# Kernel tuning notes

Hardware: AMD Instinct MI355X
Metric: run time of the kernel (lower is better)

The kernel has to match this reference:

```python
import jax, jax.numpy as jnp
import numpy as np

NEG_BIG = -9e15
ALPHA = 0.2  # LeakyReLU negative slope


def setup_inputs() -> dict:
    key = jax.random.key(0)
    k1, k2, k3, k4 = jax.random.split(key, 4)
    N, Fin, Fout = 8192, 256, 256
    input_ = jax.random.normal(k1, (N, Fin), dtype=jnp.float32)
    adj = jax.random.randint(k2, (N, N), 0, 2, dtype=jnp.int32)
    # xavier_uniform with gain=1.414
    limW = 1.414 * np.sqrt(6.0 / (Fin + Fout))
    W = jax.random.uniform(k3, (Fin, Fout), minval=-limW, maxval=limW, dtype=jnp.float32)
    lima = 1.414 * np.sqrt(6.0 / (2 * Fout + 1))
    a = jax.random.uniform(k4, (2 * Fout, 1), minval=-lima, maxval=lima, dtype=jnp.float32)
    return {"input_": input_, "adj": adj, "W": W, "a": a}


def reference(input_, adj, W, a):
    # h: [N, F]
    h = input_ @ W
    F = h.shape[1]
    # Decompose cat([h_i, h_j]) @ a into per-node projections summed by broadcast
    src = h @ a[:F, 0]   # [N]  contribution of row node i
    dst = h @ a[F:, 0]   # [N]  contribution of col node j
    e = jax.nn.leaky_relu(src[:, None] + dst[None, :], negative_slope=ALPHA)  # [N, N]
    e = jnp.where(adj > 0, e, NEG_BIG)
    attention = jax.nn.softmax(e, axis=1)
    h_prime = attention @ h  # [N, F]
    return jax.nn.relu(h_prime)  # concat=True
```

## Files before the change

### kernel.cpp

```cpp
#include <hip/hip_runtime.h>
#include <math.h>

#define NN 8192
#define FF 256
#define ALPHA 0.2f
#define JT 32
#define LP 40

typedef __bf16 bf16x8 __attribute__((ext_vector_type(8)));
typedef float  f32x4  __attribute__((ext_vector_type(4)));

__global__ __launch_bounds__(256) void k1_xw(const float* __restrict__ X,
                                             const float* __restrict__ W,
                                             float* __restrict__ h) {
    __shared__ float xs[32][FF];
    const int t = threadIdx.x;
    const int i0 = blockIdx.x * 32;
    #pragma unroll
    for (int it = 0; it < 8; ++it) {
        int f = it * 256 + t;
        int r = f >> 6;
        int c4 = (f & 63) << 2;
        *(float4*)&xs[r][c4] = *(const float4*)&X[(size_t)(i0 + r) * FF + c4];
    }
    __syncthreads();
    float acc[32];
    #pragma unroll
    for (int r = 0; r < 32; ++r) acc[r] = 0.f;
    for (int kt = 0; kt < FF; kt += 8) {
        float wk[8];
        #pragma unroll
        for (int u = 0; u < 8; ++u) wk[u] = W[(size_t)(kt + u) * FF + t];
        #pragma unroll
        for (int r = 0; r < 32; ++r) {
            float4 xa = *(float4*)&xs[r][kt];
            float4 xb = *(float4*)&xs[r][kt + 4];
            acc[r] += xa.x * wk[0] + xa.y * wk[1] + xa.z * wk[2] + xa.w * wk[3]
                    + xb.x * wk[4] + xb.y * wk[5] + xb.z * wk[6] + xb.w * wk[7];
        }
    }
    #pragma unroll
    for (int r = 0; r < 32; ++r) h[(size_t)(i0 + r) * FF + t] = acc[r];
}

__global__ __launch_bounds__(256) void k1b_split(const float* __restrict__ h,
                                                 __bf16* __restrict__ hT) {
    __shared__ float ts[64][65];
    const int t = threadIdx.x;
    const int j0 = blockIdx.x * 64;
    const int f0 = blockIdx.y * 64;
    #pragma unroll
    for (int r = 0; r < 4; ++r) {
        int jr = r * 16 + (t >> 4);
        int fc = (t & 15) * 4;
        *(float4*)&ts[jr][fc] = *(const float4*)&h[(size_t)(j0 + jr) * FF + f0 + fc];
    }
    __syncthreads();
    const int f = t >> 2;
    const int jc = (t & 3) * 16;
    union { bf16x8 v[2]; __bf16 e[16]; } hi, lo;
    #pragma unroll
    for (int u = 0; u < 16; ++u) {
        float x = ts[jc + u][f];
        __bf16 h1 = (__bf16)x;
        hi.e[u] = h1;
        lo.e[u] = (__bf16)(x - (float)h1);
    }
    size_t base = (size_t)(f0 + f) * NN + j0 + jc;
    *(bf16x8*)&hT[base]     = hi.v[0];
    *(bf16x8*)&hT[base + 8] = hi.v[1];
    size_t lbase = (size_t)FF * NN + base;
    *(bf16x8*)&hT[lbase]     = lo.v[0];
    *(bf16x8*)&hT[lbase + 8] = lo.v[1];
}

__global__ __launch_bounds__(256) void k2_srcdst(const float* __restrict__ h,
                                                 const float* __restrict__ a,
                                                 float* __restrict__ src,
                                                 float* __restrict__ dst) {
    const int wv = threadIdx.x >> 6;
    const int l = threadIdx.x & 63;
    const int i = blockIdx.x * 4 + wv;
    float s = 0.f, d = 0.f;
    #pragma unroll
    for (int k = 0; k < 4; ++k) {
        float hv = h[(size_t)i * FF + l + 64 * k];
        s += hv * a[l + 64 * k];
        d += hv * a[FF + l + 64 * k];
    }
    #pragma unroll
    for (int off = 32; off > 0; off >>= 1) {
        s += __shfl_down(s, off);
        d += __shfl_down(d, off);
    }
    if (l == 0) { src[i] = s; dst[i] = d; }
}

__global__ __launch_bounds__(256) void k2b_max(const float* __restrict__ dst,
                                               float* __restrict__ maxd) {
    __shared__ float red[256];
    float m = -1e30f;
    for (int i = threadIdx.x; i < NN; i += 256) m = fmaxf(m, dst[i]);
    red[threadIdx.x] = m;
    __syncthreads();
    for (int s = 128; s > 0; s >>= 1) {
        if (threadIdx.x < s) red[threadIdx.x] = fmaxf(red[threadIdx.x], red[threadIdx.x + s]);
        __syncthreads();
    }
    if (threadIdx.x == 0) maxd[0] = red[0];
}

__global__ __launch_bounds__(256) void k3_attn(const int* __restrict__ adj,
                                               const __bf16* __restrict__ hT,
                                               const float* __restrict__ src,
                                               const float* __restrict__ dst,
                                               const float* __restrict__ maxd,
                                               float* __restrict__ num,
                                               float* __restrict__ den,
                                               int S) {
    __shared__ __bf16 bh[2][FF][LP];
    __shared__ __bf16 wA[64][LP];
    __shared__ float dl[64][4];
    const int t = threadIdx.x;
    const int nIt = NN / 64;
    const int it = blockIdx.x % nIt;
    const int seg = blockIdx.x / nIt;
    const int i0 = it * 64;
    const int jseg = NN / S;
    const int jbeg = seg * jseg;
    const int p_i = t >> 2;
    const int p_q = t & 3;
    const float maxdv = maxd[0];
    const float src_r = src[i0 + p_i];
    const float e0 = src_r + maxdv;
    const float m_r = e0 > 0.f ? e0 : ALPHA * e0;
    float den_reg = 0.f;
    const int wv = t >> 6;
    const int l = t & 63;
    const int ln = l & 15;
    const int g = l >> 4;
    f32x4 acc[4][4];
    #pragma unroll
    for (int mt = 0; mt < 4; ++mt)
        #pragma unroll
        for (int nt = 0; nt < 4; ++nt)
            acc[mt][nt] = (f32x4){0.f, 0.f, 0.f, 0.f};

    for (int jt = 0; jt < jseg; jt += JT) {
        const int j0 = jbeg + jt;
        __syncthreads();
        #pragma unroll
        for (int r = 0; r < 8; ++r) {
            int c = t + r * 256;
            int jc = c & 3;
            int f = (c >> 2) & 255;
            int hl = c >> 10;
            bf16x8 v = *(const bf16x8*)&hT[((size_t)hl * FF + f) * NN + j0 + jc * 8];
            *(bf16x8*)&bh[hl][f][jc * 8] = v;
        }
        {
            const int* ap = adj + (size_t)(i0 + p_i) * NN + j0 + p_q * 8;
            const int4 a0 = *(const int4*)ap;
            const int4 a1 = *(const int4*)(ap + 4);
            const float* dp = dst + j0 + p_q * 8;
            const float4 d0 = *(const float4*)dp;
            const float4 d1 = *(const float4*)(dp + 4);
            const int av[8] = {a0.x, a0.y, a0.z, a0.w, a1.x, a1.y, a1.z, a1.w};
            const float dv[8] = {d0.x, d0.y, d0.z, d0.w, d1.x, d1.y, d1.z, d1.w};
            union { bf16x8 v; __bf16 e[8]; } wu;
            #pragma unroll
            for (int u = 0; u < 8; ++u) {
                float e = src_r + dv[u];
                e = e > 0.f ? e : ALPHA * e;
                float w = (av[u] > 0) ? __expf(e - m_r) : 0.f;
                den_reg += w;
                wu.e[u] = (__bf16)w;
            }
            *(bf16x8*)&wA[p_i][p_q * 8] = wu.v;
        }
        __syncthreads();
        bf16x8 af[4];
        #pragma unroll
        for (int mt = 0; mt < 4; ++mt) af[mt] = *(bf16x8*)&wA[mt * 16 + ln][g * 8];
        #pragma unroll
        for (int nt = 0; nt < 4; ++nt) {
            #pragma unroll
            for (int hl = 0; hl < 2; ++hl) {
                bf16x8 bfr = *(bf16x8*)&bh[hl][wv * 64 + nt * 16 + ln][g * 8];
                #pragma unroll
                for (int mt = 0; mt < 4; ++mt)
                    acc[mt][nt] = __builtin_amdgcn_mfma_f32_16x16x32_bf16(
                        af[mt], bfr, acc[mt][nt], 0, 0, 0);
            }
        }
    }
    #pragma unroll
    for (int mt = 0; mt < 4; ++mt)
        #pragma unroll
        for (int nt = 0; nt < 4; ++nt)
            #pragma unroll
            for (int rg = 0; rg < 4; ++rg)
                num[((size_t)seg * NN + i0 + mt * 16 + g * 4 + rg) * FF
                    + wv * 64 + nt * 16 + ln] = acc[mt][nt][rg];
    dl[p_i][p_q] = den_reg;
    __syncthreads();
    if (t < 64) den[(size_t)seg * NN + i0 + t] = dl[t][0] + dl[t][1] + dl[t][2] + dl[t][3];
}

__global__ __launch_bounds__(256) void k4_out(const float* __restrict__ num,
                                              const float* __restrict__ den,
                                              float* __restrict__ out, int S) {
    size_t f4 = (size_t)blockIdx.x * 256 + threadIdx.x;
    int i = (int)(f4 >> 6);
    int c4 = (int)(f4 & 63) << 2;
    float4 s = make_float4(0.f, 0.f, 0.f, 0.f);
    float d = 0.f;
    for (int sg = 0; sg < S; ++sg) {
        float4 v = *(const float4*)&num[((size_t)sg * NN + i) * FF + c4];
        s.x += v.x; s.y += v.y; s.z += v.z; s.w += v.w;
        d += den[(size_t)sg * NN + i];
    }
    float inv = 1.f / d;
    float4 o;
    o.x = fmaxf(s.x * inv, 0.f);
    o.y = fmaxf(s.y * inv, 0.f);
    o.z = fmaxf(s.z * inv, 0.f);
    o.w = fmaxf(s.w * inv, 0.f);
    *(float4*)&out[(size_t)i * FF + c4] = o;
}

extern "C" void kernel_launch(void* const* d_in, const int* in_sizes, int n_in,
                              void* d_out, int out_size, void* d_ws, size_t ws_size,
                              hipStream_t stream) {
    const float* X  = (const float*)d_in[0];
    const int*  adj = (const int*)d_in[1];
    const float* W  = (const float*)d_in[2];
    const float* a  = (const float*)d_in[3];
    float* out = (float*)d_out;
    char* ws = (char*)d_ws;

    const size_t off_h    = 0;
    const size_t off_hT   = off_h + (size_t)NN * FF * 4;
    const size_t off_src  = off_hT + (size_t)2 * FF * NN * 2;
    const size_t off_dst  = off_src + (size_t)NN * 4;
    const size_t off_maxd = off_dst + (size_t)NN * 4;
    const size_t off_num  = off_maxd + 256;

    int S = 8;
    while (S > 1) {
        size_t need = off_num + (size_t)S * NN * FF * 4 + (size_t)S * NN * 4;
        if (need <= ws_size) break;
        S >>= 1;
    }
    const size_t off_den = off_num + (size_t)S * NN * FF * 4;

    float* h_ws   = (float*)(ws + off_h);
    __bf16* hT_ws = (__bf16*)(ws + off_hT);
    float* src_ws = (float*)(ws + off_src);
    float* dst_ws = (float*)(ws + off_dst);
    float* maxd   = (float*)(ws + off_maxd);
    float* num_ws = (float*)(ws + off_num);
    float* den_ws = (float*)(ws + off_den);

    k1_xw<<<NN / 32, 256, 0, stream>>>(X, W, h_ws);
    k1b_split<<<dim3(NN / 64, FF / 64), 256, 0, stream>>>(h_ws, hT_ws);
    k2_srcdst<<<NN / 4, 256, 0, stream>>>(h_ws, a, src_ws, dst_ws);
    k2b_max<<<1, 256, 0, stream>>>(dst_ws, maxd);
    k3_attn<<<(NN / 64) * S, 256, 0, stream>>>(adj, hT_ws, src_ws, dst_ws, maxd,
                                               num_ws, den_ws, S);
    k4_out<<<(NN * FF / 4) / 256, 256, 0, stream>>>(num_ws, den_ws, out, S);
}
```

Measured before the change: 540.7 us.

## Fuse projection into MFMA kernel and double-buffer attention loads via LDS DMA

Replaces the scalar XW matmul, the transpose/split and the src/dst kernels with one kernel. It computes h using split-bf16 MFMA and emits hT, src and dst directly. The attention kernel now double-buffers hT tiles in LDS through global_load_lds with a swizzled layout, prefetches the adjacency and dst values for the next step, and fixes the split count at 4 with launch_bounds occupancy 2. The aim is to remove extra launches, the fp32 round trip of h and load latency in the main loop. In exchange, the fixed split count ignores the workspace size, and the bf16 three-term projection changes numerics slightly.

Measured after the change: 481.9 us. 1.12x faster.

```diff
diff --git a/kernel.cpp b/kernel.cpp
--- a/kernel.cpp
+++ b/kernel.cpp
@@ -4,103 +4,178 @@
 #define NN 8192
 #define FF 256
 #define ALPHA 0.2f
-#define JT 32
-#define LP 40
+#define SS 4
+#define JSEG (NN / SS)
+#define STEPS (JSEG / 32)
 
 typedef __bf16 bf16x8 __attribute__((ext_vector_type(8)));
+typedef __bf16 bf16x4 __attribute__((ext_vector_type(4)));
 typedef float  f32x4  __attribute__((ext_vector_type(4)));
 
-__global__ __launch_bounds__(256) void k1_xw(const float* __restrict__ X,
-                                             const float* __restrict__ W,
-                                             float* __restrict__ h) {
-    __shared__ float xs[32][FF];
-    const int t = threadIdx.x;
-    const int i0 = blockIdx.x * 32;
-    #pragma unroll
-    for (int it = 0; it < 8; ++it) {
-        int f = it * 256 + t;
-        int r = f >> 6;
-        int c4 = (f & 63) << 2;
-        *(float4*)&xs[r][c4] = *(const float4*)&X[(size_t)(i0 + r) * FF + c4];
-    }
-    __syncthreads();
-    float acc[32];
-    #pragma unroll
-    for (int r = 0; r < 32; ++r) acc[r] = 0.f;
-    for (int kt = 0; kt < FF; kt += 8) {
-        float wk[8];
-        #pragma unroll
-        for (int u = 0; u < 8; ++u) wk[u] = W[(size_t)(kt + u) * FF + t];
-        #pragma unroll
-        for (int r = 0; r < 32; ++r) {
-            float4 xa = *(float4*)&xs[r][kt];
-            float4 xb = *(float4*)&xs[r][kt + 4];
-            acc[r] += xa.x * wk[0] + xa.y * wk[1] + xa.z * wk[2] + xa.w * wk[3]
-                    + xb.x * wk[4] + xb.y * wk[5] + xb.z * wk[6] + xb.w * wk[7];
-        }
-    }
-    #pragma unroll
-    for (int r = 0; r < 32; ++r) h[(size_t)(i0 + r) * FF + t] = acc[r];
-}
-
-__global__ __launch_bounds__(256) void k1b_split(const float* __restrict__ h,
-                                                 __bf16* __restrict__ hT) {
+__device__ __forceinline__ void dma16(const void* g, void* l) {
+    __builtin_amdgcn_global_load_lds((const __attribute__((address_space(1))) void*)g,
+                                     (__attribute__((address_space(3))) void*)l,
+                                     16, 0, 0);
+}
+
+__global__ __launch_bounds__(256) void k0_wt(const float* __restrict__ W,
+                                             __bf16* __restrict__ WT) {
     __shared__ float ts[64][65];
     const int t = threadIdx.x;
-    const int j0 = blockIdx.x * 64;
-    const int f0 = blockIdx.y * 64;
+    const int k0 = blockIdx.x * 64;
+    const int n0 = blockIdx.y * 64;
     #pragma unroll
     for (int r = 0; r < 4; ++r) {
-        int jr = r * 16 + (t >> 4);
-        int fc = (t & 15) * 4;
-        *(float4*)&ts[jr][fc] = *(const float4*)&h[(size_t)(j0 + jr) * FF + f0 + fc];
+        int krow = r * 16 + (t >> 4);
+        int nc4 = (t & 15) * 4;
+        *(float4*)&ts[krow][nc4] = *(const float4*)&W[(size_t)(k0 + krow) * FF + n0 + nc4];
     }
     __syncthreads();
-    const int f = t >> 2;
-    const int jc = (t & 3) * 16;
+    const int nloc = t >> 2;
+    const int kc = (t & 3) * 16;
     union { bf16x8 v[2]; __bf16 e[16]; } hi, lo;
     #pragma unroll
     for (int u = 0; u < 16; ++u) {
-        float x = ts[jc + u][f];
+        float x = ts[kc + u][nloc];
         __bf16 h1 = (__bf16)x;
         hi.e[u] = h1;
         lo.e[u] = (__bf16)(x - (float)h1);
     }
-    size_t base = (size_t)(f0 + f) * NN + j0 + jc;
-    *(bf16x8*)&hT[base]     = hi.v[0];
-    *(bf16x8*)&hT[base + 8] = hi.v[1];
-    size_t lbase = (size_t)FF * NN + base;
-    *(bf16x8*)&hT[lbase]     = lo.v[0];
-    *(bf16x8*)&hT[lbase + 8] = lo.v[1];
-}
-
-__global__ __launch_bounds__(256) void k2_srcdst(const float* __restrict__ h,
-                                                 const float* __restrict__ a,
-                                                 float* __restrict__ src,
-                                                 float* __restrict__ dst) {
-    const int wv = threadIdx.x >> 6;
-    const int l = threadIdx.x & 63;
-    const int i = blockIdx.x * 4 + wv;
-    float s = 0.f, d = 0.f;
-    #pragma unroll
-    for (int k = 0; k < 4; ++k) {
-        float hv = h[(size_t)i * FF + l + 64 * k];
-        s += hv * a[l + 64 * k];
-        d += hv * a[FF + l + 64 * k];
-    }
-    #pragma unroll
-    for (int off = 32; off > 0; off >>= 1) {
-        s += __shfl_down(s, off);
-        d += __shfl_down(d, off);
-    }
-    if (l == 0) { src[i] = s; dst[i] = d; }
+    size_t base = (size_t)(n0 + nloc) * FF + k0 + kc;
+    *(bf16x8*)&WT[base] = hi.v[0];
+    *(bf16x8*)&WT[base + 8] = hi.v[1];
+    size_t lbase = (size_t)FF * FF + base;
+    *(bf16x8*)&WT[lbase] = lo.v[0];
+    *(bf16x8*)&WT[lbase + 8] = lo.v[1];
+}
+
+__global__ __launch_bounds__(256) void k1_h(const float* __restrict__ X,
+                                            const __bf16* __restrict__ WT,
+                                            const float* __restrict__ a,
+                                            __bf16* __restrict__ hT,
+                                            float* __restrict__ src,
+                                            float* __restrict__ dst) {
+    __shared__ __bf16 ax[2][32][40];
+    __shared__ float hs[32][264];
+    __shared__ float red[2][4][32];
+    const int t = threadIdx.x;
+    const int i0 = blockIdx.x * 32;
+    const int l = t & 63, wv = t >> 6, ln = l & 15, g = l >> 4;
+    f32x4 acc[2][4];
+    #pragma unroll
+    for (int mt = 0; mt < 2; ++mt)
+        #pragma unroll
+        for (int nt = 0; nt < 4; ++nt)
+            acc[mt][nt] = (f32x4){0.f, 0.f, 0.f, 0.f};
+
+    for (int ks = 0; ks < 8; ++ks) {
+        const int k0 = ks * 32;
+        {
+            int row = t >> 3, c4 = (t & 7) * 4;
+            float4 xv = *(const float4*)&X[(size_t)(i0 + row) * FF + k0 + c4];
+            bf16x4 hi4, lo4;
+            float xs_[4] = {xv.x, xv.y, xv.z, xv.w};
+            #pragma unroll
+            for (int u = 0; u < 4; ++u) {
+                __bf16 h1 = (__bf16)xs_[u];
+                hi4[u] = h1;
+                lo4[u] = (__bf16)(xs_[u] - (float)h1);
+            }
+            *(bf16x4*)&ax[0][row][c4] = hi4;
+            *(bf16x4*)&ax[1][row][c4] = lo4;
+        }
+        __syncthreads();
+        bf16x8 ah[2], al[2];
+        ah[0] = *(bf16x8*)&ax[0][ln][g * 8];
+        ah[1] = *(bf16x8*)&ax[0][16 + ln][g * 8];
+        al[0] = *(bf16x8*)&ax[1][ln][g * 8];
+        al[1] = *(bf16x8*)&ax[1][16 + ln][g * 8];
+        #pragma unroll
+        for (int nt = 0; nt < 4; ++nt) {
+            const int n = wv * 64 + nt * 16 + ln;
+            bf16x8 bh8 = *(const bf16x8*)&WT[(size_t)n * FF + k0 + g * 8];
+            bf16x8 bl8 = *(const bf16x8*)&WT[(size_t)(FF + n) * FF + k0 + g * 8];
+            #pragma unroll
+            for (int mt = 0; mt < 2; ++mt) {
+                acc[mt][nt] = __builtin_amdgcn_mfma_f32_16x16x32_bf16(ah[mt], bh8, acc[mt][nt], 0, 0, 0);
+                acc[mt][nt] = __builtin_amdgcn_mfma_f32_16x16x32_bf16(ah[mt], bl8, acc[mt][nt], 0, 0, 0);
+                acc[mt][nt] = __builtin_amdgcn_mfma_f32_16x16x32_bf16(al[mt], bh8, acc[mt][nt], 0, 0, 0);
+            }
+        }
+        __syncthreads();
+    }
+    float an[4], ad[4];
+    #pragma unroll
+    for (int nt = 0; nt < 4; ++nt) {
+        an[nt] = a[wv * 64 + nt * 16 + ln];
+        ad[nt] = a[FF + wv * 64 + nt * 16 + ln];
+    }
+    float sp[2][4], dp[2][4];
+    #pragma unroll
+    for (int mt = 0; mt < 2; ++mt)
+        #pragma unroll
+        for (int rg = 0; rg < 4; ++rg) { sp[mt][rg] = 0.f; dp[mt][rg] = 0.f; }
+    #pragma unroll
+    for (int mt = 0; mt < 2; ++mt)
+        #pragma unroll
+        for (int nt = 0; nt < 4; ++nt)
+            #pragma unroll
+            for (int rg = 0; rg < 4; ++rg) {
+                float v = acc[mt][nt][rg];
+                hs[mt * 16 + g * 4 + rg][wv * 64 + nt * 16 + ln] = v;
+                sp[mt][rg] += v * an[nt];
+                dp[mt][rg] += v * ad[nt];
+            }
+    #pragma unroll
+    for (int mk = 1; mk < 16; mk <<= 1)
+        #pragma unroll
+        for (int mt = 0; mt < 2; ++mt)
+            #pragma unroll
+            for (int rg = 0; rg < 4; ++rg) {
+                sp[mt][rg] += __shfl_xor(sp[mt][rg], mk);
+                dp[mt][rg] += __shfl_xor(dp[mt][rg], mk);
+            }
+    if (ln == 0) {
+        #pragma unroll
+        for (int mt = 0; mt < 2; ++mt)
+            #pragma unroll
+            for (int rg = 0; rg < 4; ++rg) {
+                red[0][wv][mt * 16 + g * 4 + rg] = sp[mt][rg];
+                red[1][wv][mt * 16 + g * 4 + rg] = dp[mt][rg];
+            }
+    }
+    __syncthreads();
+    if (t < 32) {
+        src[i0 + t] = red[0][0][t] + red[0][1][t] + red[0][2][t] + red[0][3][t];
+        dst[i0 + t] = red[1][0][t] + red[1][1][t] + red[1][2][t] + red[1][3][t];
+    }
+    {
+        const int f = t;
+        #pragma unroll
+        for (int jc = 0; jc < 4; ++jc) {
+            union { bf16x8 v; __bf16 e[8]; } hi, lo;
+            #pragma unroll
+            for (int u = 0; u < 8; ++u) {
+                float x = hs[jc * 8 + u][f];
+                __bf16 h1 = (__bf16)x;
+                hi.e[u] = h1;
+                lo.e[u] = (__bf16)(x - (float)h1);
+            }
+            *(bf16x8*)&hT[(size_t)f * NN + i0 + jc * 8] = hi.v;
+            *(bf16x8*)&hT[(size_t)(FF + f) * NN + i0 + jc * 8] = lo.v;
+        }
+    }
 }
 
 __global__ __launch_bounds__(256) void k2b_max(const float* __restrict__ dst,
                                                float* __restrict__ maxd) {
     __shared__ float red[256];
     float m = -1e30f;
-    for (int i = threadIdx.x; i < NN; i += 256) m = fmaxf(m, dst[i]);
+    #pragma unroll
+    for (int r = 0; r < NN / 1024; ++r) {
+        float4 v = *(const float4*)&dst[(r * 256 + threadIdx.x) * 4];
+        m = fmaxf(m, fmaxf(fmaxf(v.x, v.y), fmaxf(v.z, v.w)));
+    }
     red[threadIdx.x] = m;
     __syncthreads();
     for (int s = 128; s > 0; s >>= 1) {
@@ -110,35 +185,51 @@
     if (threadIdx.x == 0) maxd[0] = red[0];
 }
 
-__global__ __launch_bounds__(256) void k3_attn(const int* __restrict__ adj,
-                                               const __bf16* __restrict__ hT,
-                                               const float* __restrict__ src,
-                                               const float* __restrict__ dst,
-                                               const float* __restrict__ maxd,
-                                               float* __restrict__ num,
-                                               float* __restrict__ den,
-                                               int S) {
-    __shared__ __bf16 bh[2][FF][LP];
-    __shared__ __bf16 wA[64][LP];
+__global__ __launch_bounds__(256, 2) void k3_attn(const int* __restrict__ adj,
+                                                  const __bf16* __restrict__ hT,
+                                                  const float* __restrict__ src,
+                                                  const float* __restrict__ dst,
+                                                  const float* __restrict__ maxd,
+                                                  float* __restrict__ num,
+                                                  float* __restrict__ den) {
+    __shared__ __bf16 bh[2][2048 * 8];
+    __shared__ __bf16 wA[2][64][40];
     __shared__ float dl[64][4];
     const int t = threadIdx.x;
-    const int nIt = NN / 64;
-    const int it = blockIdx.x % nIt;
-    const int seg = blockIdx.x / nIt;
+    const int l = t & 63, wv = t >> 6, ln = l & 15, g = l >> 4;
+    const int it = blockIdx.x & 127;
+    const int seg = blockIdx.x >> 7;
     const int i0 = it * 64;
-    const int jseg = NN / S;
-    const int jbeg = seg * jseg;
-    const int p_i = t >> 2;
-    const int p_q = t & 3;
+    const int jbeg = seg * JSEG;
+    const int p_i = t >> 2, p_q = t & 3;
     const float maxdv = maxd[0];
     const float src_r = src[i0 + p_i];
     const float e0 = src_r + maxdv;
     const float m_r = e0 > 0.f ? e0 : ALPHA * e0;
+
+    int rowbase[8], cb[8];
+    #pragma unroll
+    for (int r = 0; r < 8; ++r) {
+        int cbase = r * 256 + wv * 64;
+        int c = cbase + l;
+        int hl = c >> 10;
+        int f = (c >> 2) & 255;
+        int pc = c & 3;
+        int jc = pc ^ ((f >> 1) & 3);
+        rowbase[r] = (hl * FF + f) * NN + jc * 8;
+        cb[r] = __builtin_amdgcn_readfirstlane(cbase);
+    }
+    const int* arow = adj + (size_t)(i0 + p_i) * NN + p_q * 8;
+
+    #pragma unroll
+    for (int r = 0; r < 8; ++r)
+        dma16(&hT[rowbase[r] + jbeg], &bh[0][cb[r] * 8]);
+    int4 a0 = *(const int4*)(arow + jbeg);
+    int4 a1 = *(const int4*)(arow + jbeg + 4);
+    float4 d0 = *(const float4*)&dst[jbeg + p_q * 8];
+    float4 d1 = *(const float4*)&dst[jbeg + p_q * 8 + 4];
+
     float den_reg = 0.f;
-    const int wv = t >> 6;
-    const int l = t & 63;
-    const int ln = l & 15;
-    const int g = l >> 4;
     f32x4 acc[4][4];
     #pragma unroll
     for (int mt = 0; mt < 4; ++mt)
@@ -146,25 +237,9 @@
         for (int nt = 0; nt < 4; ++nt)
             acc[mt][nt] = (f32x4){0.f, 0.f, 0.f, 0.f};
 
-    for (int jt = 0; jt < jseg; jt += JT) {
-        const int j0 = jbeg + jt;
-        __syncthreads();
-        #pragma unroll
-        for (int r = 0; r < 8; ++r) {
-            int c = t + r * 256;
-            int jc = c & 3;
-            int f = (c >> 2) & 255;
-            int hl = c >> 10;
-            bf16x8 v = *(const bf16x8*)&hT[((size_t)hl * FF + f) * NN + j0 + jc * 8];
-            *(bf16x8*)&bh[hl][f][jc * 8] = v;
-        }
+    for (int s = 0; s < STEPS; ++s) {
+        const int cur = s & 1;
         {
-            const int* ap = adj + (size_t)(i0 + p_i) * NN + j0 + p_q * 8;
-            const int4 a0 = *(const int4*)ap;
-            const int4 a1 = *(const int4*)(ap + 4);
-            const float* dp = dst + j0 + p_q * 8;
-            const float4 d0 = *(const float4*)dp;
-            const float4 d1 = *(const float4*)(dp + 4);
             const int av[8] = {a0.x, a0.y, a0.z, a0.w, a1.x, a1.y, a1.z, a1.w};
             const float dv[8] = {d0.x, d0.y, d0.z, d0.w, d1.x, d1.y, d1.z, d1.w};
             union { bf16x8 v; __bf16 e[8]; } wu;
@@ -176,17 +251,31 @@
                 den_reg += w;
                 wu.e[u] = (__bf16)w;
             }
-            *(bf16x8*)&wA[p_i][p_q * 8] = wu.v;
+            *(bf16x8*)&wA[cur][p_i][p_q * 8] = wu.v;
         }
         __syncthreads();
+        if (s + 1 < STEPS) {
+            const int j1 = jbeg + (s + 1) * 32;
+            #pragma unroll
+            for (int r = 0; r < 8; ++r)
+                dma16(&hT[rowbase[r] + j1], &bh[cur ^ 1][cb[r] * 8]);
+            a0 = *(const int4*)(arow + j1);
+            a1 = *(const int4*)(arow + j1 + 4);
+            d0 = *(const float4*)&dst[j1 + p_q * 8];
+            d1 = *(const float4*)&dst[j1 + p_q * 8 + 4];
+        }
         bf16x8 af[4];
         #pragma unroll
-        for (int mt = 0; mt < 4; ++mt) af[mt] = *(bf16x8*)&wA[mt * 16 + ln][g * 8];
+        for (int mt = 0; mt < 4; ++mt)
+            af[mt] = *(bf16x8*)&wA[cur][mt * 16 + ln][g * 8];
         #pragma unroll
         for (int nt = 0; nt < 4; ++nt) {
+            const int f = wv * 64 + nt * 16 + ln;
+            const int sw = (f >> 1) & 3;
             #pragma unroll
             for (int hl = 0; hl < 2; ++hl) {
-                bf16x8 bfr = *(bf16x8*)&bh[hl][wv * 64 + nt * 16 + ln][g * 8];
+                const int chunk = (hl * FF + f) * 4 + (g ^ sw);
+                bf16x8 bfr = *(bf16x8*)&bh[cur][chunk * 8];
                 #pragma unroll
                 for (int mt = 0; mt < 4; ++mt)
                     acc[mt][nt] = __builtin_amdgcn_mfma_f32_16x16x32_bf16(
@@ -209,13 +298,14 @@
 
 __global__ __launch_bounds__(256) void k4_out(const float* __restrict__ num,
                                               const float* __restrict__ den,
-                                              float* __restrict__ out, int S) {
+                                              float* __restrict__ out) {
     size_t f4 = (size_t)blockIdx.x * 256 + threadIdx.x;
     int i = (int)(f4 >> 6);
     int c4 = (int)(f4 & 63) << 2;
     float4 s = make_float4(0.f, 0.f, 0.f, 0.f);
     float d = 0.f;
-    for (int sg = 0; sg < S; ++sg) {
+    #pragma unroll
+    for (int sg = 0; sg < SS; ++sg) {
         float4 v = *(const float4*)&num[((size_t)sg * NN + i) * FF + c4];
         s.x += v.x; s.y += v.y; s.z += v.z; s.w += v.w;
         d += den[(size_t)sg * NN + i];
@@ -239,34 +329,26 @@
     float* out = (float*)d_out;
     char* ws = (char*)d_ws;
 
-    const size_t off_h    = 0;
-    const size_t off_hT   = off_h + (size_t)NN * FF * 4;
-    const size_t off_src  = off_hT + (size_t)2 * FF * NN * 2;
+    const size_t off_hT   = 0;
+    const size_t off_wt   = off_hT + (size_t)2 * FF * NN * 2;
+    const size_t off_src  = off_wt + (size_t)2 * FF * FF * 2;
     const size_t off_dst  = off_src + (size_t)NN * 4;
     const size_t off_maxd = off_dst + (size_t)NN * 4;
     const size_t off_num  = off_maxd + 256;
-
-    int S = 8;
-    while (S > 1) {
-        size_t need = off_num + (size_t)S * NN * FF * 4 + (size_t)S * NN * 4;
-        if (need <= ws_size) break;
-        S >>= 1;
-    }
-    const size_t off_den = off_num + (size_t)S * NN * FF * 4;
-
-    float* h_ws   = (float*)(ws + off_h);
+    const size_t off_den  = off_num + (size_t)SS * NN * FF * 4;
+
     __bf16* hT_ws = (__bf16*)(ws + off_hT);
+    __bf16* wt_ws = (__bf16*)(ws + off_wt);
     float* src_ws = (float*)(ws + off_src);
     float* dst_ws = (float*)(ws + off_dst);
     float* maxd   = (float*)(ws + off_maxd);
     float* num_ws = (float*)(ws + off_num);
     float* den_ws = (float*)(ws + off_den);
 
-    k1_xw<<<NN / 32, 256, 0, stream>>>(X, W, h_ws);
-    k1b_split<<<dim3(NN / 64, FF / 64), 256, 0, stream>>>(h_ws, hT_ws);
-    k2_srcdst<<<NN / 4, 256, 0, stream>>>(h_ws, a, src_ws, dst_ws);
+    k0_wt<<<dim3(FF / 64, FF / 64), 256, 0, stream>>>(W, wt_ws);
+    k1_h<<<NN / 32, 256, 0, stream>>>(X, wt_ws, a, hT_ws, src_ws, dst_ws);
     k2b_max<<<1, 256, 0, stream>>>(dst_ws, maxd);
-    k3_attn<<<(NN / 64) * S, 256, 0, stream>>>(adj, hT_ws, src_ws, dst_ws, maxd,
-                                               num_ws, den_ws, S);
-    k4_out<<<(NN * FF / 4) / 256, 256, 0, stream>>>(num_ws, den_ws, out, S);
-}
+    k3_attn<<<(NN / 64) * SS, 256, 0, stream>>>(adj, hT_ws, src_ws, dst_ws, maxd,
+                                                num_ws, den_ws);
+    k4_out<<<(NN * FF / 4) / 256, 256, 0, stream>>>(num_ws, den_ws, out);
+}
```
